# Kernel tuning notes

Measured on AMD Instinct MI355X. Metric: run time of the kernel, lower is better.

## Reference

```python
import jax, jax.numpy as jnp
import numpy as np

TAU = 2.0
V_TH = 1.0
ALPHA = 2.0  # ATan surrogate alpha

@jax.custom_vjp
def spike_fn(x):
    return (x >= 0.0).astype(x.dtype)

def _spike_fwd(x):
    return spike_fn(x), x

def _spike_bwd(x, g):
    # spikingjelly ATan surrogate: alpha/2 / (1 + (pi/2*alpha*x)^2)
    return (g * (ALPHA / 2.0) / (1.0 + (jnp.pi / 2.0 * ALPHA * x) ** 2),)

spike_fn.defvjp(_spike_fwd, _spike_bwd)

def lif_step(v, h):
    # decay_input=True, v_reset=0: v += (h - v)/tau
    v = v + (h - v) / TAU
    s = spike_fn(v - V_TH)
    v = v * (1.0 - s)  # hard reset to v_reset=0
    return v, s

def setup_inputs() -> dict:
    key = jax.random.key(0)
    k1, k2, k3 = jax.random.split(key, 3)
    B, T, I, H, O = 128, 2048, 128, 1024, 128
    x = jax.random.normal(k1, (B, T, I), dtype=jnp.float32)
    W1 = jax.random.normal(k2, (H, I), dtype=jnp.float32) / np.sqrt(I)
    b1 = jnp.zeros((H,), dtype=jnp.float32)
    W2 = jax.random.normal(k3, (O, H), dtype=jnp.float32) / np.sqrt(H)
    b2 = jnp.zeros((O,), dtype=jnp.float32)
    return {"x": x, "W1": W1, "b1": b1, "W2": W2, "b2": b2}

def reference(x, W1, b1, W2, b2):
    B, T, I = x.shape
    H = W1.shape[0]
    O = W2.shape[0]
    xt = jnp.transpose(x, (1, 0, 2))  # [T, B, I]

    def step(carry, x_t):
        v1, v2 = carry
        h1 = x_t @ W1.T + b1
        v1, s1 = lif_step(v1, h1)
        h2 = s1 @ W2.T + b2
        v2, s2 = lif_step(v2, h2)
        return (v1, v2), s2

    v1_0 = jnp.zeros((B, H), dtype=x.dtype)
    v2_0 = jnp.zeros((B, O), dtype=x.dtype)
    _, outs = jax.lax.scan(step, (v1_0, v2_0), xt)  # [T, B, O]
    decision_start = T // 2
    return jnp.sum(outs[decision_start:], axis=0)  # [B, O]
```

## Files before the change

### kernel.cpp

```cpp
#include <hip/hip_runtime.h>
#include <stdint.h>

#define NB 128
#define NT 2048
#define NI 128
#define NH 1024
#define NO 128

typedef float f32x4 __attribute__((ext_vector_type(4)));
typedef float f32x16 __attribute__((ext_vector_type(16)));

__global__ __launch_bounds__(256) void w2p_kernel(
    const float* __restrict__ W2, float2* __restrict__ W2P)
{
    const int idx = blockIdx.x * 256 + threadIdx.x;
    const int k = idx >> 6;
    const int j = idx & 63;
    W2P[idx] = make_float2(W2[(size_t)j * NH + k], W2[(size_t)(j + 64) * NH + k]);
}

#define WLQ(V, OFF)                                                       \
    asm volatile("global_load_dwordx4 %0, %1, off offset:" #OFF          \
                 : "=v"(V) : "v"(wp))

#define Q4(WQ, XV, J)                                                     \
    do {                                                                  \
        a0 = fmaf(WQ.x, (XV)[(J) + 0], a0);                               \
        a1 = fmaf(WQ.y, (XV)[(J) + 1], a1);                               \
        a2 = fmaf(WQ.z, (XV)[(J) + 2], a2);                               \
        a3 = fmaf(WQ.w, (XV)[(J) + 3], a3);                               \
    } while (0)

__global__ __launch_bounds__(256, 4) void snn_phaseA(
    const float* __restrict__ x, const float* __restrict__ W1,
    const float* __restrict__ b1, uint64_t* __restrict__ s1bits)
{
    const int b = blockIdx.x >> 4;
    const int hg = blockIdx.x & 15;
    const int kq = __builtin_amdgcn_readfirstlane(threadIdx.x >> 6);
    const int lane = threadIdx.x & 63;
    const int h = hg * 64 + lane;

    f32x4 wq0, wq1, wq2, wq3, wq4, wq5, wq6, wq7;
    const float* wp = W1 + (size_t)h * NI + kq * 32;
    WLQ(wq0, 0);  WLQ(wq1, 16); WLQ(wq2, 32);  WLQ(wq3, 48);
    WLQ(wq4, 64); WLQ(wq5, 80); WLQ(wq6, 96);  WLQ(wq7, 112);
    asm volatile("s_waitcnt vmcnt(0)"
                 : "+v"(wq0), "+v"(wq1), "+v"(wq2), "+v"(wq3),
                   "+v"(wq4), "+v"(wq5), "+v"(wq6), "+v"(wq7)
                 :
                 : "memory");
    __builtin_amdgcn_sched_barrier(0);

    const float bias = b1[h];
    __shared__ float red[2][3][64];

    const float* __restrict__ xb = x + (size_t)b * NT * NI + kq * 32;
    uint64_t* s1w = s1bits + (size_t)b * (NH / 64) + hg;

    float v = 0.0f;
#pragma unroll 1
    for (int t = 0; t < NT; ++t) {
        const float* xr = xb + (size_t)t * NI;
        f32x16 xlo, xhi;
        asm volatile("s_load_dwordx16 %0, %1, 0x0"  : "=s"(xlo) : "s"(xr));
        asm volatile("s_load_dwordx16 %0, %1, 0x40" : "=s"(xhi) : "s"(xr));
        asm volatile("s_waitcnt lgkmcnt(0)" : "+s"(xlo), "+s"(xhi));
        __builtin_amdgcn_sched_barrier(0);

        float a0 = 0.f, a1 = 0.f, a2 = 0.f, a3 = 0.f;
        Q4(wq0, xlo, 0);  Q4(wq1, xlo, 4);  Q4(wq2, xlo, 8);  Q4(wq3, xlo, 12);
        Q4(wq4, xhi, 0);  Q4(wq5, xhi, 4);  Q4(wq6, xhi, 8);  Q4(wq7, xhi, 12);
        const float partial = (a0 + a1) + (a2 + a3);

        if (kq) red[t & 1][kq - 1][lane] = partial;
        __syncthreads();
        if (!kq) {
            const float r0 = red[t & 1][0][lane];
            const float r1 = red[t & 1][1][lane];
            const float r2 = red[t & 1][2][lane];
            const float h1 = ((partial + r0) + (r1 + r2)) + bias;
            v = fmaf(h1 - v, 0.5f, v);
            const bool sp = (v >= 1.0f);
            v = sp ? 0.0f : v;
            const unsigned long long m = __ballot(sp);
            if (lane == 0) *s1w = (uint64_t)m;
        }
        s1w += NB * (NH / 64);
    }
}

__global__ __launch_bounds__(256, 4) void snn_phaseB(
    const uint64_t* __restrict__ s1bits, const float2* __restrict__ W2P,
    float* __restrict__ h2)
{
    const int wv = threadIdx.x >> 6;
    const int lane = threadIdx.x & 63;
    const size_t m = (size_t)blockIdx.x * 4 + wv;

    const uint64_t* __restrict__ sb = s1bits + m * (NH / 64);
    float a0 = 0.f, a1 = 0.f;

#pragma unroll 1
    for (int wd = 0; wd < NH / 64; ++wd) {
        const uint64_t m64 = sb[wd];
        const uint32_t mlo = (uint32_t)__builtin_amdgcn_readfirstlane((int)(uint32_t)m64);
        const uint32_t mhi = (uint32_t)__builtin_amdgcn_readfirstlane((int)(uint32_t)(m64 >> 32));
        uint64_t msk = ((uint64_t)mhi << 32) | mlo;
        while (msk) {
            const int i = __builtin_ctzll(msk);
            msk &= (msk - 1);
            const size_t k = ((size_t)wd << 6) + i;
            const float2 ww = W2P[k * 64 + lane];
            a0 += ww.x;
            a1 += ww.y;
        }
    }
    h2[m * NO + lane] = a0;
    h2[m * NO + 64 + lane] = a1;
}

__global__ __launch_bounds__(64) void snn_phaseD(
    const float* __restrict__ h2, const float* __restrict__ b2,
    float* __restrict__ out)
{
    const int idx = blockIdx.x * 64 + threadIdx.x;
    const int b = idx >> 7;
    const int o = idx & 127;
    const float bias = b2[o];

    const float* __restrict__ p = h2 + (size_t)b * NO + o;
    float v = 0.f, c = 0.f;
#pragma unroll 16
    for (int t = 0; t < NT; ++t) {
        const float hh = p[(size_t)t * NB * NO] + bias;
        v = fmaf(hh - v, 0.5f, v);
        const bool s = (v >= 1.0f);
        v = s ? 0.f : v;
        if (t >= NT / 2) c += s ? 1.f : 0.f;
    }
    out[idx] = c;
}

extern "C" void kernel_launch(void* const* d_in, const int* in_sizes, int n_in,
                              void* d_out, int out_size, void* d_ws,
                              size_t ws_size, hipStream_t stream)
{
    const float* x  = (const float*)d_in[0];
    const float* W1 = (const float*)d_in[1];
    const float* b1 = (const float*)d_in[2];
    const float* W2 = (const float*)d_in[3];
    const float* b2 = (const float*)d_in[4];
    float* out = (float*)d_out;

    uint8_t* ws = (uint8_t*)d_ws;
    uint64_t* s1bits = (uint64_t*)ws;
    float2* W2P = (float2*)(ws + (size_t)NT * NB * (NH / 64) * 8);
    float* h2 = (float*)(ws + (size_t)NT * NB * (NH / 64) * 8 +
                         (size_t)NH * 64 * sizeof(float2));

    w2p_kernel<<<dim3((NH * 64) / 256), dim3(256), 0, stream>>>(W2, W2P);
    snn_phaseA<<<dim3(NB * 16), dim3(256), 0, stream>>>(x, W1, b1, s1bits);
    snn_phaseB<<<dim3((NT * NB) / 4), dim3(256), 0, stream>>>(s1bits, W2P, h2);
    snn_phaseD<<<dim3(256), dim3(64), 0, stream>>>(h2, b2, out);
}
```

Baseline: 2.093 ms.

## Process four batch rows per phase-A block with 8-way K split

Phase A now assigns four batch rows and 64 hidden units to each 512-thread block. The K dimension is split across 8 waves of 16 inputs each, so every wave keeps only 16 weights in registers and reuses them across four batch rows. The LDS reduction grows to 8 partials per row, and the first four waves each finish the LIF update for one batch row. The aim is to cut per-step overhead from the barrier and scalar loads, amortised over more work, and to use fewer, larger blocks. The cost is a larger sync domain and 512 blocks that might not fill the GPU evenly.

After: 4.137 ms. +97.6%, slower.

```diff
diff --git a/kernel.cpp b/kernel.cpp
--- a/kernel.cpp
+++ b/kernel.cpp
@@ -19,67 +19,91 @@
     W2P[idx] = make_float2(W2[(size_t)j * NH + k], W2[(size_t)(j + 64) * NH + k]);
 }
 
-#define WLQ(V, OFF)                                                       \
-    asm volatile("global_load_dwordx4 %0, %1, off offset:" #OFF          \
-                 : "=v"(V) : "v"(wp))
-
-#define Q4(WQ, XV, J)                                                     \
+#define Q4(WQ, XV, J, A0, A1, A2, A3)                                     \
     do {                                                                  \
-        a0 = fmaf(WQ.x, (XV)[(J) + 0], a0);                               \
-        a1 = fmaf(WQ.y, (XV)[(J) + 1], a1);                               \
-        a2 = fmaf(WQ.z, (XV)[(J) + 2], a2);                               \
-        a3 = fmaf(WQ.w, (XV)[(J) + 3], a3);                               \
+        A0 = fmaf(WQ.x, (XV)[(J) + 0], A0);                               \
+        A1 = fmaf(WQ.y, (XV)[(J) + 1], A1);                               \
+        A2 = fmaf(WQ.z, (XV)[(J) + 2], A2);                               \
+        A3 = fmaf(WQ.w, (XV)[(J) + 3], A3);                               \
     } while (0)
 
-__global__ __launch_bounds__(256, 4) void snn_phaseA(
+__global__ __launch_bounds__(512, 4) void snn_phaseA(
     const float* __restrict__ x, const float* __restrict__ W1,
     const float* __restrict__ b1, uint64_t* __restrict__ s1bits)
 {
-    const int b = blockIdx.x >> 4;
+    const int bq = blockIdx.x >> 4;
     const int hg = blockIdx.x & 15;
     const int kq = __builtin_amdgcn_readfirstlane(threadIdx.x >> 6);
     const int lane = threadIdx.x & 63;
     const int h = hg * 64 + lane;
+    const int b0 = bq * 4;
 
-    f32x4 wq0, wq1, wq2, wq3, wq4, wq5, wq6, wq7;
-    const float* wp = W1 + (size_t)h * NI + kq * 32;
-    WLQ(wq0, 0);  WLQ(wq1, 16); WLQ(wq2, 32);  WLQ(wq3, 48);
-    WLQ(wq4, 64); WLQ(wq5, 80); WLQ(wq6, 96);  WLQ(wq7, 112);
-    asm volatile("s_waitcnt vmcnt(0)"
-                 : "+v"(wq0), "+v"(wq1), "+v"(wq2), "+v"(wq3),
-                   "+v"(wq4), "+v"(wq5), "+v"(wq6), "+v"(wq7)
-                 :
-                 : "memory");
-    __builtin_amdgcn_sched_barrier(0);
+    const f32x4* __restrict__ wqp =
+        reinterpret_cast<const f32x4*>(W1 + (size_t)h * NI + kq * 16);
+    const f32x4 w0 = wqp[0], w1 = wqp[1], w2 = wqp[2], w3 = wqp[3];
 
     const float bias = b1[h];
-    __shared__ float red[2][3][64];
+    __shared__ float red[2][8][4][64];
 
-    const float* __restrict__ xb = x + (size_t)b * NT * NI + kq * 32;
-    uint64_t* s1w = s1bits + (size_t)b * (NH / 64) + hg;
+    const float* __restrict__ xr0 = x + (size_t)(b0 + 0) * NT * NI + kq * 16;
+    const float* __restrict__ xr1 = x + (size_t)(b0 + 1) * NT * NI + kq * 16;
+    const float* __restrict__ xr2 = x + (size_t)(b0 + 2) * NT * NI + kq * 16;
+    const float* __restrict__ xr3 = x + (size_t)(b0 + 3) * NT * NI + kq * 16;
+
+    uint64_t* s1w =
+        s1bits + (size_t)(b0 + kq) * (NH / 64) + hg;
 
     float v = 0.0f;
 #pragma unroll 1
     for (int t = 0; t < NT; ++t) {
-        const float* xr = xb + (size_t)t * NI;
-        f32x16 xlo, xhi;
-        asm volatile("s_load_dwordx16 %0, %1, 0x0"  : "=s"(xlo) : "s"(xr));
-        asm volatile("s_load_dwordx16 %0, %1, 0x40" : "=s"(xhi) : "s"(xr));
-        asm volatile("s_waitcnt lgkmcnt(0)" : "+s"(xlo), "+s"(xhi));
+        f32x16 x0, x1, x2, x3;
+        asm volatile("s_load_dwordx16 %0, %1, 0x0" : "=s"(x0) : "s"(xr0));
+        asm volatile("s_load_dwordx16 %0, %1, 0x0" : "=s"(x1) : "s"(xr1));
+        asm volatile("s_load_dwordx16 %0, %1, 0x0" : "=s"(x2) : "s"(xr2));
+        asm volatile("s_load_dwordx16 %0, %1, 0x0" : "=s"(x3) : "s"(xr3));
+        asm volatile("s_waitcnt lgkmcnt(0)"
+                     : "+s"(x0), "+s"(x1), "+s"(x2), "+s"(x3));
         __builtin_amdgcn_sched_barrier(0);
 
-        float a0 = 0.f, a1 = 0.f, a2 = 0.f, a3 = 0.f;
-        Q4(wq0, xlo, 0);  Q4(wq1, xlo, 4);  Q4(wq2, xlo, 8);  Q4(wq3, xlo, 12);
-        Q4(wq4, xhi, 0);  Q4(wq5, xhi, 4);  Q4(wq6, xhi, 8);  Q4(wq7, xhi, 12);
-        const float partial = (a0 + a1) + (a2 + a3);
+        float a00 = 0.f, a01 = 0.f, a02 = 0.f, a03 = 0.f;
+        float a10 = 0.f, a11 = 0.f, a12 = 0.f, a13 = 0.f;
+        float a20 = 0.f, a21 = 0.f, a22 = 0.f, a23 = 0.f;
+        float a30 = 0.f, a31 = 0.f, a32 = 0.f, a33 = 0.f;
+        Q4(w0, x0, 0, a00, a01, a02, a03);
+        Q4(w1, x0, 4, a00, a01, a02, a03);
+        Q4(w2, x0, 8, a00, a01, a02, a03);
+        Q4(w3, x0, 12, a00, a01, a02, a03);
+        Q4(w0, x1, 0, a10, a11, a12, a13);
+        Q4(w1, x1, 4, a10, a11, a12, a13);
+        Q4(w2, x1, 8, a10, a11, a12, a13);
+        Q4(w3, x1, 12, a10, a11, a12, a13);
+        Q4(w0, x2, 0, a20, a21, a22, a23);
+        Q4(w1, x2, 4, a20, a21, a22, a23);
+        Q4(w2, x2, 8, a20, a21, a22, a23);
+        Q4(w3, x2, 12, a20, a21, a22, a23);
+        Q4(w0, x3, 0, a30, a31, a32, a33);
+        Q4(w1, x3, 4, a30, a31, a32, a33);
+        Q4(w2, x3, 8, a30, a31, a32, a33);
+        Q4(w3, x3, 12, a30, a31, a32, a33);
 
-        if (kq) red[t & 1][kq - 1][lane] = partial;
+        const int par = t & 1;
+        red[par][kq][0][lane] = (a00 + a01) + (a02 + a03);
+        red[par][kq][1][lane] = (a10 + a11) + (a12 + a13);
+        red[par][kq][2][lane] = (a20 + a21) + (a22 + a23);
+        red[par][kq][3][lane] = (a30 + a31) + (a32 + a33);
         __syncthreads();
-        if (!kq) {
-            const float r0 = red[t & 1][0][lane];
-            const float r1 = red[t & 1][1][lane];
-            const float r2 = red[t & 1][2][lane];
-            const float h1 = ((partial + r0) + (r1 + r2)) + bias;
+
+        if (kq < 4) {
+            const float r0 = red[par][0][kq][lane];
+            const float r1 = red[par][1][kq][lane];
+            const float r2 = red[par][2][kq][lane];
+            const float r3 = red[par][3][kq][lane];
+            const float r4 = red[par][4][kq][lane];
+            const float r5 = red[par][5][kq][lane];
+            const float r6 = red[par][6][kq][lane];
+            const float r7 = red[par][7][kq][lane];
+            const float h1 =
+                (((r0 + r1) + (r2 + r3)) + ((r4 + r5) + (r6 + r7))) + bias;
             v = fmaf(h1 - v, 0.5f, v);
             const bool sp = (v >= 1.0f);
             v = sp ? 0.0f : v;
@@ -87,6 +111,7 @@
             if (lane == 0) *s1w = (uint64_t)m;
         }
         s1w += NB * (NH / 64);
+        xr0 += NI; xr1 += NI; xr2 += NI; xr3 += NI;
     }
 }
 
@@ -160,7 +185,7 @@
                          (size_t)NH * 64 * sizeof(float2));
 
     w2p_kernel<<<dim3((NH * 64) / 256), dim3(256), 0, stream>>>(W2, W2P);
-    snn_phaseA<<<dim3(NB * 16), dim3(256), 0, stream>>>(x, W1, b1, s1bits);
+    snn_phaseA<<<dim3(512), dim3(512), 0, stream>>>(x, W1, b1, s1bits);
     snn_phaseB<<<dim3((NT * NB) / 4), dim3(256), 0, stream>>>(s1bits, W2P, h2);
     snn_phaseD<<<dim3(256), dim3(64), 0, stream>>>(h2, b2, out);
 }
```

## Process four timesteps per barrier in phase A with W1 staged in LDS

Applied to the files above, without the earlier changes.

Phase A now handles four timesteps per loop iteration. The cross-wave partial-sum reduction and its __syncthreads happen once per four steps instead of once per step, and the x loads for four rows are issued together as scalar loads. Each wave's W1 slice moves from registers into a padded LDS tile and is reread from LDS every step, which adds LDS traffic and raises LDS use per block in exchange for fewer barriers and more memory-level parallelism. The LIF update still runs serially per step on wave 0.

Result: slower. 2.319 ms (+10.8%).

```diff
diff --git a/kernel.cpp b/kernel.cpp
--- a/kernel.cpp
+++ b/kernel.cpp
@@ -19,19 +19,55 @@
     W2P[idx] = make_float2(W2[(size_t)j * NH + k], W2[(size_t)(j + 64) * NH + k]);
 }
 
-#define WLQ(V, OFF)                                                       \
-    asm volatile("global_load_dwordx4 %0, %1, off offset:" #OFF          \
-                 : "=v"(V) : "v"(wp))
+#define XL(DST, IMM)                                                      \
+    asm volatile("s_load_dwordx16 %0, %1, " #IMM : "=s"(DST) : "s"(xb))
 
-#define Q4(WQ, XV, J)                                                     \
+#define F16(ACC, XV)                                                      \
     do {                                                                  \
-        a0 = fmaf(WQ.x, (XV)[(J) + 0], a0);                               \
-        a1 = fmaf(WQ.y, (XV)[(J) + 1], a1);                               \
-        a2 = fmaf(WQ.z, (XV)[(J) + 2], a2);                               \
-        a3 = fmaf(WQ.w, (XV)[(J) + 3], a3);                               \
+        ACC = fmaf(w0.x, (XV)[0],  ACC);                                  \
+        ACC = fmaf(w0.y, (XV)[1],  ACC);                                  \
+        ACC = fmaf(w0.z, (XV)[2],  ACC);                                  \
+        ACC = fmaf(w0.w, (XV)[3],  ACC);                                  \
+        ACC = fmaf(w1.x, (XV)[4],  ACC);                                  \
+        ACC = fmaf(w1.y, (XV)[5],  ACC);                                  \
+        ACC = fmaf(w1.z, (XV)[6],  ACC);                                  \
+        ACC = fmaf(w1.w, (XV)[7],  ACC);                                  \
+        ACC = fmaf(w2.x, (XV)[8],  ACC);                                  \
+        ACC = fmaf(w2.y, (XV)[9],  ACC);                                  \
+        ACC = fmaf(w2.z, (XV)[10], ACC);                                  \
+        ACC = fmaf(w2.w, (XV)[11], ACC);                                  \
+        ACC = fmaf(w3.x, (XV)[12], ACC);                                  \
+        ACC = fmaf(w3.y, (XV)[13], ACC);                                  \
+        ACC = fmaf(w3.z, (XV)[14], ACC);                                  \
+        ACC = fmaf(w3.w, (XV)[15], ACC);                                  \
     } while (0)
 
-__global__ __launch_bounds__(256, 4) void snn_phaseA(
+#define KCHUNK(Q0, I0, I1, I2, I3)                                        \
+    {                                                                     \
+        f32x16 xv0, xv1, xv2, xv3;                                        \
+        XL(xv0, I0); XL(xv1, I1); XL(xv2, I2); XL(xv3, I3);               \
+        asm volatile("s_waitcnt lgkmcnt(0)"                               \
+                     : "+s"(xv0), "+s"(xv1), "+s"(xv2), "+s"(xv3));       \
+        const f32x4 w0 = wrow[(Q0) + 0];                                  \
+        const f32x4 w1 = wrow[(Q0) + 1];                                  \
+        const f32x4 w2 = wrow[(Q0) + 2];                                  \
+        const f32x4 w3 = wrow[(Q0) + 3];                                  \
+        F16(t0, xv0); F16(t1, xv1); F16(t2, xv2); F16(t3, xv3);           \
+    }
+
+#define LIFSTEP(TT, TACC)                                                 \
+    {                                                                     \
+        const float h1 = ((TACC + red[par][0][TT][lane]) +                \
+                          (red[par][1][TT][lane] + red[par][2][TT][lane])) + \
+                         bias;                                            \
+        v = fmaf(h1 - v, 0.5f, v);                                        \
+        const bool sp = (v >= 1.0f);                                      \
+        v = sp ? 0.0f : v;                                                \
+        const unsigned long long m = __ballot(sp);                        \
+        if (lane == 0) s1w[(size_t)TT * NB * (NH / 64)] = (uint64_t)m;    \
+    }
+
+__global__ __launch_bounds__(256, 4) void snn_phaseA4(
     const float* __restrict__ x, const float* __restrict__ W1,
     const float* __restrict__ b1, uint64_t* __restrict__ s1bits)
 {
@@ -41,52 +77,49 @@
     const int lane = threadIdx.x & 63;
     const int h = hg * 64 + lane;
 
-    f32x4 wq0, wq1, wq2, wq3, wq4, wq5, wq6, wq7;
-    const float* wp = W1 + (size_t)h * NI + kq * 32;
-    WLQ(wq0, 0);  WLQ(wq1, 16); WLQ(wq2, 32);  WLQ(wq3, 48);
-    WLQ(wq4, 64); WLQ(wq5, 80); WLQ(wq6, 96);  WLQ(wq7, 112);
-    asm volatile("s_waitcnt vmcnt(0)"
-                 : "+v"(wq0), "+v"(wq1), "+v"(wq2), "+v"(wq3),
-                   "+v"(wq4), "+v"(wq5), "+v"(wq6), "+v"(wq7)
-                 :
-                 : "memory");
-    __builtin_amdgcn_sched_barrier(0);
+    __shared__ f32x4 wlds[64][33];
+    __shared__ float red[2][3][4][64];
+
+#pragma unroll
+    for (int i = 0; i < 8; ++i) {
+        const int c = threadIdx.x + i * 256;
+        const int r = c >> 5;
+        const int kc = c & 31;
+        wlds[r][kc] = *reinterpret_cast<const f32x4*>(
+            W1 + (size_t)(hg * 64 + r) * NI + kc * 4);
+    }
+    __syncthreads();
 
     const float bias = b1[h];
-    __shared__ float red[2][3][64];
+    const f32x4* __restrict__ wrow = &wlds[lane][0];
+    const int wb = kq * 8;
 
-    const float* __restrict__ xb = x + (size_t)b * NT * NI + kq * 32;
+    const float* xb = x + (size_t)b * NT * NI + kq * 32;
     uint64_t* s1w = s1bits + (size_t)b * (NH / 64) + hg;
 
     float v = 0.0f;
 #pragma unroll 1
-    for (int t = 0; t < NT; ++t) {
-        const float* xr = xb + (size_t)t * NI;
-        f32x16 xlo, xhi;
-        asm volatile("s_load_dwordx16 %0, %1, 0x0"  : "=s"(xlo) : "s"(xr));
-        asm volatile("s_load_dwordx16 %0, %1, 0x40" : "=s"(xhi) : "s"(xr));
-        asm volatile("s_waitcnt lgkmcnt(0)" : "+s"(xlo), "+s"(xhi));
-        __builtin_amdgcn_sched_barrier(0);
+    for (int tc = 0; tc < NT; tc += 4) {
+        float t0 = 0.f, t1 = 0.f, t2 = 0.f, t3 = 0.f;
+        KCHUNK(wb + 0, 0x0,  0x200, 0x400, 0x600);
+        KCHUNK(wb + 4, 0x40, 0x240, 0x440, 0x640);
 
-        float a0 = 0.f, a1 = 0.f, a2 = 0.f, a3 = 0.f;
-        Q4(wq0, xlo, 0);  Q4(wq1, xlo, 4);  Q4(wq2, xlo, 8);  Q4(wq3, xlo, 12);
-        Q4(wq4, xhi, 0);  Q4(wq5, xhi, 4);  Q4(wq6, xhi, 8);  Q4(wq7, xhi, 12);
-        const float partial = (a0 + a1) + (a2 + a3);
-
-        if (kq) red[t & 1][kq - 1][lane] = partial;
+        const int par = (tc >> 2) & 1;
+        if (kq) {
+            red[par][kq - 1][0][lane] = t0;
+            red[par][kq - 1][1][lane] = t1;
+            red[par][kq - 1][2][lane] = t2;
+            red[par][kq - 1][3][lane] = t3;
+        }
         __syncthreads();
         if (!kq) {
-            const float r0 = red[t & 1][0][lane];
-            const float r1 = red[t & 1][1][lane];
-            const float r2 = red[t & 1][2][lane];
-            const float h1 = ((partial + r0) + (r1 + r2)) + bias;
-            v = fmaf(h1 - v, 0.5f, v);
-            const bool sp = (v >= 1.0f);
-            v = sp ? 0.0f : v;
-            const unsigned long long m = __ballot(sp);
-            if (lane == 0) *s1w = (uint64_t)m;
+            LIFSTEP(0, t0);
+            LIFSTEP(1, t1);
+            LIFSTEP(2, t2);
+            LIFSTEP(3, t3);
         }
-        s1w += NB * (NH / 64);
+        s1w += (size_t)4 * NB * (NH / 64);
+        xb += 4 * NI;
     }
 }
 
@@ -160,7 +193,7 @@
                          (size_t)NH * 64 * sizeof(float2));
 
     w2p_kernel<<<dim3((NH * 64) / 256), dim3(256), 0, stream>>>(W2, W2P);
-    snn_phaseA<<<dim3(NB * 16), dim3(256), 0, stream>>>(x, W1, b1, s1bits);
+    snn_phaseA4<<<dim3(NB * 16), dim3(256), 0, stream>>>(x, W1, b1, s1bits);
     snn_phaseB<<<dim3((NT * NB) / 4), dim3(256), 0, stream>>>(s1bits, W2P, h2);
     snn_phaseD<<<dim3(256), dim3(64), 0, stream>>>(h2, b2, out);
 }
```
